# Performance work log

Hardware: AMD Instinct MI355X
Metric: run time of the kernel (lower is better)

## Reference

```python
import jax, jax.numpy as jnp
import numpy as np


def setup_inputs() -> dict:
    key = jax.random.key(0)
    k1, k2, k3, k4 = jax.random.split(key, 4)
    B, S, IN, OUT = 4, 512, 4096, 11008
    x = jax.random.normal(k1, (B, S, IN), dtype=jnp.float32)
    # int8-valued weights stored as int32 (symmetric per-output-channel quant)
    w_int8 = jax.random.randint(k2, (OUT, IN), -128, 128, dtype=jnp.int32)
    # per-output-channel fp32 scales (positive, like absmax/127)
    scales = jax.random.uniform(k3, (OUT,), dtype=jnp.float32, minval=1e-4, maxval=0.05)
    bias = jax.random.normal(k4, (OUT,), dtype=jnp.float32)
    return {"x": x, "w_int8": w_int8, "scales": scales, "bias": bias}


def reference(x, w_int8, scales, bias):
    # On-the-fly dequant: w[o, i] = int8[o, i] * scale[o], then y = x @ w.T + b
    w = (w_int8.astype(jnp.float32) * scales[:, None]).astype(x.dtype)  # [OUT, IN]
    return jnp.einsum('bsi,oi->bso', x, w) + bias
```

## Files before the change

kernel.cpp:

```cpp
#include <hip/hip_runtime.h>
#include <hip/hip_bf16.h>
#include <stdint.h>


typedef __attribute__((ext_vector_type(8))) short short8;
typedef __attribute__((ext_vector_type(4))) float f32x4;
typedef __attribute__((ext_vector_type(4))) float float4v;
typedef __attribute__((ext_vector_type(4))) int int4v;

#define MM 2048
#define NN 11008
#define KK 4096
#define NT (KK / 128)
#define ROWB ((size_t)KK)

static __device__ __forceinline__ ushort f2bf_rne(float f) {
    uint32_t u = __builtin_bit_cast(uint32_t, f);
    u = (u + 0x7FFFu + ((u >> 16) & 1u)) >> 16;
    return (ushort)u;
}
static __device__ __forceinline__ ushort i2bf_exact(int v) {
    return (ushort)(__builtin_bit_cast(uint32_t, (float)v) >> 16);
}
static __device__ __forceinline__ void gload16(const void* g, void* lds) {
    __builtin_amdgcn_global_load_lds(
        (const __attribute__((address_space(1))) uint32_t*)g,
        (__attribute__((address_space(3))) uint32_t*)lds, 16, 0, 0);
}

#define BAR() do { asm volatile("" ::: "memory"); __builtin_amdgcn_s_barrier(); asm volatile("" ::: "memory"); } while (0)

__global__ __launch_bounds__(256)
void rowmax_x(const float* __restrict__ X, float* __restrict__ Sx, float* __restrict__ SxInv) {
    const int r = blockIdx.x;
    const float4v* xr = (const float4v*)(X + (size_t)r * KK);
    float m = 0.f;
    for (int i = threadIdx.x; i < KK / 4; i += 256) {
        float4v v = xr[i];
        m = fmaxf(m, fmaxf(fmaxf(fabsf(v[0]), fabsf(v[1])),
                           fmaxf(fabsf(v[2]), fabsf(v[3]))));
    }
#pragma unroll
    for (int off = 32; off; off >>= 1) m = fmaxf(m, __shfl_down(m, off));
    __shared__ float wmax[4];
    if ((threadIdx.x & 63) == 0) wmax[threadIdx.x >> 6] = m;
    __syncthreads();
    if (threadIdx.x == 0) {
        float a = fmaxf(fmaxf(wmax[0], wmax[1]), fmaxf(wmax[2], wmax[3]));
        Sx[r]    = a / 127.f;
        SxInv[r] = (a > 0.f) ? 127.f / a : 0.f;
    }
}

__global__ __launch_bounds__(256)
void quant_pack(const float* __restrict__ X, const int* __restrict__ W,
                const float* __restrict__ SxInv,
                char* __restrict__ Xq, char* __restrict__ Wq) {
    const int NX4 = MM * KK / 4;
    const int NW4 = NN * KK / 4;
    const int stride = gridDim.x * blockDim.x;
    for (int i = blockIdx.x * blockDim.x + threadIdx.x; i < NX4 + NW4; i += stride) {
        if (i < NX4) {
            float4v v = ((const float4v*)X)[i];
            const float inv = SxInv[i >> 10];
            uint32_t p = 0;
#pragma unroll
            for (int j = 0; j < 4; ++j) {
                int q = (int)rintf(v[j] * inv);
                p |= ((uint32_t)(q & 255)) << (8 * j);
            }
            ((uint32_t*)Xq)[i] = p;
        } else {
            int j = i - NX4;
            int4v w = ((const int4v*)W)[j];
            uint32_t p = ((uint32_t)(w[0] & 255)) | ((uint32_t)(w[1] & 255) << 8) |
                         ((uint32_t)(w[2] & 255) << 16) | ((uint32_t)(w[3] & 255) << 24);
            ((uint32_t*)Wq)[j] = p;
        }
    }
}

static __device__ __forceinline__ void stage_half(const char* g, char* lhalf,
                                                  int wid, size_t ktbyte) {
    const char* s = g + ktbyte;
    char* l = lhalf + wid * 1024;
    gload16(s, l);
    gload16(s + (size_t)64 * ROWB, l + 8192);
}

__global__ __launch_bounds__(512, 2)
void gemm_256_i8(const char* __restrict__ A, const char* __restrict__ B,
                 const float* __restrict__ Sx, const float* __restrict__ S,
                 const float* __restrict__ Bv, float* __restrict__ Y) {
    __shared__ char smem[131072];
    char* bufA0 = smem;
    char* bufB0 = smem + 32768;
    char* bufA1 = smem + 65536;
    char* bufB1 = smem + 98304;

    const int tid  = threadIdx.x;
    const int lane = tid & 63;
    const int wid  = tid >> 6;
    const int wm   = wid >> 2;
    const int wn   = wid & 3;
    const int l15  = lane & 15;
    const int q    = lane >> 4;
    const int s7   = lane & 7;

    const int swz  = (blockIdx.x & 7) * 43 + (blockIdx.x >> 3);
    const int brow = (swz & 7) * 256;
    const int bcol = (swz >> 3) * 256;

    const int srow  = tid >> 3;
    const int sslot = (tid & 7) ^ (srow & 7);
    const char* gA0 = A + (size_t)(brow + srow) * ROWB + sslot * 16;
    const char* gA1 = gA0 + (size_t)128 * ROWB;
    const char* gB0 = B + (size_t)(bcol + srow) * ROWB + sslot * 16;
    const char* gB1 = gB0 + (size_t)128 * ROWB;

    const int rdA = (wm * 128 + l15) * 128;
    const int rdB = (wn * 64  + l15) * 128;
    const int k0  = ((q * 16)      ^ (s7 << 4));
    const int k1  = ((64 + q * 16) ^ (s7 << 4));

#define LDA(buf, m, koff) (*(const int4v*)((buf) + rdA + (m) * 2048 + (koff)))
#define LDB(buf, n, koff) (*(const int4v*)((buf) + rdB + (n) * 2048 + (koff)))

    int4v acc[8][4] = {};

    stage_half(gA0, bufA0,         wid, 0);
    stage_half(gA1, bufA0 + 16384, wid, 0);
    stage_half(gB0, bufB0,         wid, 0);
    stage_half(gB1, bufB0 + 16384, wid, 0);
    stage_half(gA0, bufA1,         wid, 128);
    asm volatile("s_waitcnt vmcnt(2)" ::: "memory");
    BAR();

    char* curA = bufA0; char* curB = bufB0;
    char* nxtA = bufA1; char* nxtB = bufB1;

    for (int t = 0; t < NT; ++t) {
        const size_t kb1 = (size_t)((t + 1 < NT) ? t + 1 : NT - 1) * 128;
        const size_t kb2 = (size_t)((t + 2 < NT) ? t + 2 : NT - 1) * 128;

        int4v af[4][2], bf[4][2];

#pragma unroll
        for (int m = 0; m < 4; ++m) { af[m][0] = LDA(curA, m, k0); af[m][1] = LDA(curA, m, k1); }
#pragma unroll
        for (int n = 0; n < 2; ++n) { bf[n][0] = LDB(curB, n, k0); bf[n][1] = LDB(curB, n, k1); }
        stage_half(gA1, nxtA + 16384, wid, kb1);
        BAR();
        __builtin_amdgcn_s_setprio(1);
#pragma unroll
        for (int m = 0; m < 4; ++m)
#pragma unroll
            for (int n = 0; n < 2; ++n) {
                acc[m][n] = __builtin_amdgcn_mfma_i32_16x16x64_i8(af[m][0], bf[n][0], acc[m][n], 0, 0, 0);
                acc[m][n] = __builtin_amdgcn_mfma_i32_16x16x64_i8(af[m][1], bf[n][1], acc[m][n], 0, 0, 0);
            }
        __builtin_amdgcn_s_setprio(0);
        BAR();

#pragma unroll
        for (int n = 2; n < 4; ++n) { bf[n][0] = LDB(curB, n, k0); bf[n][1] = LDB(curB, n, k1); }
        stage_half(gB0, nxtB, wid, kb1);
        BAR();
        __builtin_amdgcn_s_setprio(1);
#pragma unroll
        for (int m = 0; m < 4; ++m)
#pragma unroll
            for (int n = 2; n < 4; ++n) {
                acc[m][n] = __builtin_amdgcn_mfma_i32_16x16x64_i8(af[m][0], bf[n][0], acc[m][n], 0, 0, 0);
                acc[m][n] = __builtin_amdgcn_mfma_i32_16x16x64_i8(af[m][1], bf[n][1], acc[m][n], 0, 0, 0);
            }
        __builtin_amdgcn_s_setprio(0);
        BAR();

#pragma unroll
        for (int m = 0; m < 4; ++m) { af[m][0] = LDA(curA, m + 4, k0); af[m][1] = LDA(curA, m + 4, k1); }
        stage_half(gB1, nxtB + 16384, wid, kb1);
        BAR();
        __builtin_amdgcn_s_setprio(1);
#pragma unroll
        for (int m = 0; m < 4; ++m)
#pragma unroll
            for (int n = 0; n < 2; ++n) {
                acc[m + 4][n] = __builtin_amdgcn_mfma_i32_16x16x64_i8(af[m][0], bf[n][0], acc[m + 4][n], 0, 0, 0);
                acc[m + 4][n] = __builtin_amdgcn_mfma_i32_16x16x64_i8(af[m][1], bf[n][1], acc[m + 4][n], 0, 0, 0);
            }
        __builtin_amdgcn_s_setprio(0);
        BAR();

        stage_half(gA0, curA, wid, kb2);
        BAR();
        __builtin_amdgcn_s_setprio(1);
#pragma unroll
        for (int m = 0; m < 4; ++m)
#pragma unroll
            for (int n = 2; n < 4; ++n) {
                acc[m + 4][n] = __builtin_amdgcn_mfma_i32_16x16x64_i8(af[m][0], bf[n][0], acc[m + 4][n], 0, 0, 0);
                acc[m + 4][n] = __builtin_amdgcn_mfma_i32_16x16x64_i8(af[m][1], bf[n][1], acc[m + 4][n], 0, 0, 0);
            }
        __builtin_amdgcn_s_setprio(0);
        asm volatile("s_waitcnt vmcnt(2)" ::: "memory");
        BAR();

        char* tA = curA; curA = nxtA; nxtA = tA;
        char* tB = curB; curB = nxtB; nxtB = tB;
    }

#pragma unroll
    for (int n = 0; n < 4; ++n) {
        const int gc = bcol + wn * 64 + n * 16 + l15;
        const float sj = S[gc];
        const float bj = Bv[gc];
#pragma unroll
        for (int m = 0; m < 8; ++m) {
            const int grow = brow + wm * 128 + m * 16 + q * 4;
            float* yp = Y + (size_t)grow * NN + gc;
#pragma unroll
            for (int r = 0; r < 4; ++r)
                yp[(size_t)r * NN] = (float)acc[m][n][r] * (Sx[grow + r] * sj) + bj;
        }
    }
#undef LDA
#undef LDB
}

#define BMF 128
#define BKF 32
#define LDW (BKF + 8)
__global__ __launch_bounds__(256, 2)
void int8lin_fused(const float* __restrict__ X, const int* __restrict__ W,
                   const float* __restrict__ S, const float* __restrict__ Bv,
                   float* __restrict__ Y) {
    __shared__ ushort As[BMF][LDW];
    __shared__ ushort Bs[BMF][LDW];
    const int tid = threadIdx.x, lane = tid & 63, wid = tid >> 6;
    const int wm = wid >> 1, wn = wid & 1, l15 = lane & 15, kh = (lane >> 4) * 8;
    const int bm = blockIdx.x & 15, bn = blockIdx.x >> 4;
    const int brow = bm * BMF, bcol = bn * BMF;
    const int srow = tid >> 1, scol = (tid & 1) * 16;
    const float* xg = X + (size_t)(brow + srow) * KK + scol;
    const int*   wg = W + (size_t)(bcol + srow) * KK + scol;
    f32x4 acc[4][4] = {};
    for (int kt = 0; kt < KK / BKF; ++kt) {
        float4v x0 = *(const float4v*)(xg + 0), x1 = *(const float4v*)(xg + 4);
        float4v x2 = *(const float4v*)(xg + 8), x3 = *(const float4v*)(xg + 12);
        int4v w0 = *(const int4v*)(wg + 0), w1 = *(const int4v*)(wg + 4);
        int4v w2 = *(const int4v*)(wg + 8), w3 = *(const int4v*)(wg + 12);
        xg += BKF; wg += BKF;
        short8 xa = { (short)f2bf_rne(x0[0]), (short)f2bf_rne(x0[1]), (short)f2bf_rne(x0[2]), (short)f2bf_rne(x0[3]),
                      (short)f2bf_rne(x1[0]), (short)f2bf_rne(x1[1]), (short)f2bf_rne(x1[2]), (short)f2bf_rne(x1[3]) };
        short8 xb = { (short)f2bf_rne(x2[0]), (short)f2bf_rne(x2[1]), (short)f2bf_rne(x2[2]), (short)f2bf_rne(x2[3]),
                      (short)f2bf_rne(x3[0]), (short)f2bf_rne(x3[1]), (short)f2bf_rne(x3[2]), (short)f2bf_rne(x3[3]) };
        short8 wa = { (short)i2bf_exact(w0[0]), (short)i2bf_exact(w0[1]), (short)i2bf_exact(w0[2]), (short)i2bf_exact(w0[3]),
                      (short)i2bf_exact(w1[0]), (short)i2bf_exact(w1[1]), (short)i2bf_exact(w1[2]), (short)i2bf_exact(w1[3]) };
        short8 wb = { (short)i2bf_exact(w2[0]), (short)i2bf_exact(w2[1]), (short)i2bf_exact(w2[2]), (short)i2bf_exact(w2[3]),
                      (short)i2bf_exact(w3[0]), (short)i2bf_exact(w3[1]), (short)i2bf_exact(w3[2]), (short)i2bf_exact(w3[3]) };
        __syncthreads();
        *(short8*)&As[srow][scol] = xa; *(short8*)&As[srow][scol + 8] = xb;
        *(short8*)&Bs[srow][scol] = wa; *(short8*)&Bs[srow][scol + 8] = wb;
        __syncthreads();
        short8 af[4], bf4[4];
#pragma unroll
        for (int i = 0; i < 4; ++i) af[i] = *(const short8*)&As[wm * 64 + i * 16 + l15][kh];
#pragma unroll
        for (int j = 0; j < 4; ++j) bf4[j] = *(const short8*)&Bs[wn * 64 + j * 16 + l15][kh];
#pragma unroll
        for (int i = 0; i < 4; ++i)
#pragma unroll
            for (int j = 0; j < 4; ++j)
                acc[i][j] = __builtin_amdgcn_mfma_f32_16x16x32_bf16(af[i], bf4[j], acc[i][j], 0, 0, 0);
    }
#pragma unroll
    for (int j = 0; j < 4; ++j) {
        const int gc = bcol + wn * 64 + j * 16 + l15;
        const float sj = S[gc], bj = Bv[gc];
#pragma unroll
        for (int i = 0; i < 4; ++i) {
            const int grow = brow + wm * 64 + i * 16 + (lane >> 4) * 4;
            float* yp = Y + (size_t)grow * NN + gc;
#pragma unroll
            for (int r = 0; r < 4; ++r)
                yp[(size_t)r * NN] = acc[i][j][r] * sj + bj;
        }
    }
}

extern "C" void kernel_launch(void* const* d_in, const int* in_sizes, int n_in,
                              void* d_out, int out_size, void* d_ws, size_t ws_size,
                              hipStream_t stream) {
    const float* x = (const float*)d_in[0];
    const int*   w = (const int*)d_in[1];
    const float* s = (const float*)d_in[2];
    const float* b = (const float*)d_in[3];
    float* y = (float*)d_out;

    const size_t wq_b = (size_t)NN * KK;
    const size_t xq_b = (size_t)MM * KK;
    const size_t need = wq_b + xq_b + 2 * MM * sizeof(float) + 256;
    if (ws_size >= need) {
        char*  Wq    = (char*)d_ws;
        char*  Xq    = Wq + wq_b;
        float* Sx    = (float*)(Xq + xq_b);
        float* SxInv = Sx + MM;
        hipLaunchKernelGGL(rowmax_x,   dim3(MM),   dim3(256), 0, stream, x, Sx, SxInv);
        hipLaunchKernelGGL(quant_pack, dim3(4096), dim3(256), 0, stream, x, w, SxInv, Xq, Wq);
        hipLaunchKernelGGL(gemm_256_i8, dim3((MM / 256) * (NN / 256)), dim3(512), 0, stream,
                           Xq, Wq, Sx, s, b, y);
    } else {
        hipLaunchKernelGGL(int8lin_fused, dim3((MM / BMF) * (NN / BMF)), dim3(256), 0, stream,
                           x, w, s, b, y);
    }
}
```

Measured before the change: 176.2 us.

## Shrink int8 GEMM tile to 256x128 with BK64 and simpler double-buffered pipeline

Replaces the 256x256, K-step-128 int8 MFMA GEMM with a 256x128 tile and a K-step of 64. The launch bound moves from 2 to 4 blocks per CU, LDS drops from 128KB to 48KB per block, and each wave now owns a 64x64 sub-tile. The four barrier-separated MFMA phases per iteration become one load-compute phase with prefetch two steps ahead. The aim is to fix the poor wave quantization of 344 large blocks on the CUs, raise occupancy and cut barrier overhead. The cost is less operand reuse per loaded byte and twice as many K iterations.

```diff
diff --git a/kernel.cpp b/kernel.cpp
--- a/kernel.cpp
+++ b/kernel.cpp
@@ -11,7 +11,7 @@
 #define MM 2048
 #define NN 11008
 #define KK 4096
-#define NT (KK / 128)
+#define NT (KK / 64)
 #define ROWB ((size_t)KK)
 
 static __device__ __forceinline__ ushort f2bf_rne(float f) {
@@ -27,8 +27,6 @@
         (const __attribute__((address_space(1))) uint32_t*)g,
         (__attribute__((address_space(3))) uint32_t*)lds, 16, 0, 0);
 }
-
-#define BAR() do { asm volatile("" ::: "memory"); __builtin_amdgcn_s_barrier(); asm volatile("" ::: "memory"); } while (0)
 
 __global__ __launch_bounds__(256)
 void rowmax_x(const float* __restrict__ X, float* __restrict__ Sx, float* __restrict__ SxInv) {
@@ -80,131 +78,85 @@
     }
 }
 
-static __device__ __forceinline__ void stage_half(const char* g, char* lhalf,
-                                                  int wid, size_t ktbyte) {
-    const char* s = g + ktbyte;
-    char* l = lhalf + wid * 1024;
-    gload16(s, l);
-    gload16(s + (size_t)64 * ROWB, l + 8192);
-}
-
-__global__ __launch_bounds__(512, 2)
-void gemm_256_i8(const char* __restrict__ A, const char* __restrict__ B,
-                 const float* __restrict__ Sx, const float* __restrict__ S,
-                 const float* __restrict__ Bv, float* __restrict__ Y) {
-    __shared__ char smem[131072];
-    char* bufA0 = smem;
-    char* bufB0 = smem + 32768;
-    char* bufA1 = smem + 65536;
-    char* bufB1 = smem + 98304;
+static __device__ __forceinline__ void stageA(const char* g, char* lds, int wid, size_t kb) {
+    gload16(g + kb,                       lds + wid * 1024);
+    gload16(g + kb + (size_t)128 * ROWB,  lds + 8192 + wid * 1024);
+}
+static __device__ __forceinline__ void stageB(const char* g, char* lds, int wid, size_t kb) {
+    gload16(g + kb, lds + wid * 1024);
+}
+
+__global__ __launch_bounds__(512, 4)
+void gemm_i8(const char* __restrict__ A, const char* __restrict__ B,
+             const float* __restrict__ Sx, const float* __restrict__ S,
+             const float* __restrict__ Bv, float* __restrict__ Y) {
+    __shared__ char smem[49152];
+    char* bA0 = smem;
+    char* bA1 = smem + 16384;
+    char* bB0 = smem + 32768;
+    char* bB1 = smem + 40960;
 
     const int tid  = threadIdx.x;
     const int lane = tid & 63;
     const int wid  = tid >> 6;
-    const int wm   = wid >> 2;
-    const int wn   = wid & 3;
+    const int wm   = wid >> 1;
+    const int wn   = wid & 1;
     const int l15  = lane & 15;
     const int q    = lane >> 4;
-    const int s7   = lane & 7;
-
-    const int swz  = (blockIdx.x & 7) * 43 + (blockIdx.x >> 3);
-    const int brow = (swz & 7) * 256;
-    const int bcol = (swz >> 3) * 256;
-
-    const int srow  = tid >> 3;
-    const int sslot = (tid & 7) ^ (srow & 7);
-    const char* gA0 = A + (size_t)(brow + srow) * ROWB + sslot * 16;
-    const char* gA1 = gA0 + (size_t)128 * ROWB;
-    const char* gB0 = B + (size_t)(bcol + srow) * ROWB + sslot * 16;
-    const char* gB1 = gB0 + (size_t)128 * ROWB;
-
-    const int rdA = (wm * 128 + l15) * 128;
-    const int rdB = (wn * 64  + l15) * 128;
-    const int k0  = ((q * 16)      ^ (s7 << 4));
-    const int k1  = ((64 + q * 16) ^ (s7 << 4));
-
-#define LDA(buf, m, koff) (*(const int4v*)((buf) + rdA + (m) * 2048 + (koff)))
-#define LDB(buf, n, koff) (*(const int4v*)((buf) + rdB + (n) * 2048 + (koff)))
-
-    int4v acc[8][4] = {};
-
-    stage_half(gA0, bufA0,         wid, 0);
-    stage_half(gA1, bufA0 + 16384, wid, 0);
-    stage_half(gB0, bufB0,         wid, 0);
-    stage_half(gB1, bufB0 + 16384, wid, 0);
-    stage_half(gA0, bufA1,         wid, 128);
-    asm volatile("s_waitcnt vmcnt(2)" ::: "memory");
-    BAR();
-
-    char* curA = bufA0; char* curB = bufB0;
-    char* nxtA = bufA1; char* nxtB = bufB1;
+
+    const int swz  = (blockIdx.x & 7) * 86 + (blockIdx.x >> 3);
+    const int brow = (swz / 86) * 256;
+    const int bcol = (swz % 86) * 128;
+
+    const int srow4 = tid >> 2;
+    const int sslot = (tid & 3) ^ ((srow4 >> 1) & 3);
+    const char* gA = A + (size_t)(brow + srow4) * ROWB + sslot * 16;
+    const char* gB = B + (size_t)(bcol + srow4) * ROWB + sslot * 16;
+
+    const int rdA = (wm * 64 + l15) * 64;
+    const int rdB = (wn * 64 + l15) * 64;
+    const int kq  = (q ^ ((l15 >> 1) & 3)) * 16;
+
+#define LDA(buf, m) (*(const int4v*)((buf) + rdA + (m) * 1024 + kq))
+#define LDB(buf, n) (*(const int4v*)((buf) + rdB + (n) * 1024 + kq))
+
+    int4v acc[4][4] = {};
+
+    stageA(gA, bA0, wid, 0);
+    stageB(gB, bB0, wid, 0);
+    stageA(gA, bA1, wid, 64);
+    stageB(gB, bB1, wid, 64);
+    asm volatile("s_waitcnt vmcnt(3)" ::: "memory");
+    __builtin_amdgcn_s_barrier();
+
+    char* curA = bA0; char* curB = bB0;
+    char* nxtA = bA1; char* nxtB = bB1;
 
     for (int t = 0; t < NT; ++t) {
-        const size_t kb1 = (size_t)((t + 1 < NT) ? t + 1 : NT - 1) * 128;
-        const size_t kb2 = (size_t)((t + 2 < NT) ? t + 2 : NT - 1) * 128;
-
-        int4v af[4][2], bf[4][2];
-
-#pragma unroll
-        for (int m = 0; m < 4; ++m) { af[m][0] = LDA(curA, m, k0); af[m][1] = LDA(curA, m, k1); }
-#pragma unroll
-        for (int n = 0; n < 2; ++n) { bf[n][0] = LDB(curB, n, k0); bf[n][1] = LDB(curB, n, k1); }
-        stage_half(gA1, nxtA + 16384, wid, kb1);
-        BAR();
+        const size_t kb2 = (size_t)((t + 2 < NT) ? t + 2 : NT - 1) * 64;
+
+        int4v af[4], bf[4];
+#pragma unroll
+        for (int m = 0; m < 4; ++m) af[m] = LDA(curA, m);
+#pragma unroll
+        for (int n = 0; n < 4; ++n) bf[n] = LDB(curB, n);
+
+        asm volatile("s_waitcnt lgkmcnt(0)" ::: "memory");
+        __builtin_amdgcn_s_barrier();
+
+        stageA(gA, curA, wid, kb2);
+        stageB(gB, curB, wid, kb2);
+
         __builtin_amdgcn_s_setprio(1);
 #pragma unroll
         for (int m = 0; m < 4; ++m)
 #pragma unroll
-            for (int n = 0; n < 2; ++n) {
-                acc[m][n] = __builtin_amdgcn_mfma_i32_16x16x64_i8(af[m][0], bf[n][0], acc[m][n], 0, 0, 0);
-                acc[m][n] = __builtin_amdgcn_mfma_i32_16x16x64_i8(af[m][1], bf[n][1], acc[m][n], 0, 0, 0);
-            }
+            for (int n = 0; n < 4; ++n)
+                acc[m][n] = __builtin_amdgcn_mfma_i32_16x16x64_i8(af[m], bf[n], acc[m][n], 0, 0, 0);
         __builtin_amdgcn_s_setprio(0);
-        BAR();
-
-#pragma unroll
-        for (int n = 2; n < 4; ++n) { bf[n][0] = LDB(curB, n, k0); bf[n][1] = LDB(curB, n, k1); }
-        stage_half(gB0, nxtB, wid, kb1);
-        BAR();
-        __builtin_amdgcn_s_setprio(1);
-#pragma unroll
-        for (int m = 0; m < 4; ++m)
-#pragma unroll
-            for (int n = 2; n < 4; ++n) {
-                acc[m][n] = __builtin_amdgcn_mfma_i32_16x16x64_i8(af[m][0], bf[n][0], acc[m][n], 0, 0, 0);
-                acc[m][n] = __builtin_amdgcn_mfma_i32_16x16x64_i8(af[m][1], bf[n][1], acc[m][n], 0, 0, 0);
-            }
-        __builtin_amdgcn_s_setprio(0);
-        BAR();
-
-#pragma unroll
-        for (int m = 0; m < 4; ++m) { af[m][0] = LDA(curA, m + 4, k0); af[m][1] = LDA(curA, m + 4, k1); }
-        stage_half(gB1, nxtB + 16384, wid, kb1);
-        BAR();
-        __builtin_amdgcn_s_setprio(1);
-#pragma unroll
-        for (int m = 0; m < 4; ++m)
-#pragma unroll
-            for (int n = 0; n < 2; ++n) {
-                acc[m + 4][n] = __builtin_amdgcn_mfma_i32_16x16x64_i8(af[m][0], bf[n][0], acc[m + 4][n], 0, 0, 0);
-                acc[m + 4][n] = __builtin_amdgcn_mfma_i32_16x16x64_i8(af[m][1], bf[n][1], acc[m + 4][n], 0, 0, 0);
-            }
-        __builtin_amdgcn_s_setprio(0);
-        BAR();
-
-        stage_half(gA0, curA, wid, kb2);
-        BAR();
-        __builtin_amdgcn_s_setprio(1);
-#pragma unroll
-        for (int m = 0; m < 4; ++m)
-#pragma unroll
-            for (int n = 2; n < 4; ++n) {
-                acc[m + 4][n] = __builtin_amdgcn_mfma_i32_16x16x64_i8(af[m][0], bf[n][0], acc[m + 4][n], 0, 0, 0);
-                acc[m + 4][n] = __builtin_amdgcn_mfma_i32_16x16x64_i8(af[m][1], bf[n][1], acc[m + 4][n], 0, 0, 0);
-            }
-        __builtin_amdgcn_s_setprio(0);
-        asm volatile("s_waitcnt vmcnt(2)" ::: "memory");
-        BAR();
+
+        asm volatile("s_waitcnt vmcnt(3)" ::: "memory");
+        __builtin_amdgcn_s_barrier();
 
         char* tA = curA; curA = nxtA; nxtA = tA;
         char* tB = curB; curB = nxtB; nxtB = tB;
@@ -216,8 +168,8 @@
         const float sj = S[gc];
         const float bj = Bv[gc];
 #pragma unroll
-        for (int m = 0; m < 8; ++m) {
-            const int grow = brow + wm * 128 + m * 16 + q * 4;
+        for (int m = 0; m < 4; ++m) {
+            const int grow = brow + wm * 64 + m * 16 + q * 4;
             float* yp = Y + (size_t)grow * NN + gc;
 #pragma unroll
             for (int r = 0; r < 4; ++r)
@@ -308,7 +260,7 @@
         float* SxInv = Sx + MM;
         hipLaunchKernelGGL(rowmax_x,   dim3(MM),   dim3(256), 0, stream, x, Sx, SxInv);
         hipLaunchKernelGGL(quant_pack, dim3(4096), dim3(256), 0, stream, x, w, SxInv, Xq, Wq);
-        hipLaunchKernelGGL(gemm_256_i8, dim3((MM / 256) * (NN / 256)), dim3(512), 0, stream,
+        hipLaunchKernelGGL(gemm_i8, dim3((MM / 256) * (NN / 128)), dim3(512), 0, stream,
                            Xq, Wq, Sx, s, b, y);
     } else {
         hipLaunchKernelGGL(int8lin_fused, dim3((MM / BMF) * (NN / BMF)), dim3(256), 0, stream,
```

Measured after the change: 165.3 us. 6.2% less time.
